# Performance work log

Hardware: AMD Instinct MI355X
Metric: run time of the kernel (lower is better)

The kernel has to match this reference:

```python
import jax, jax.numpy as jnp
import numpy as np

H, W = 256, 256
N = 1024          # num gaussians
K = 4             # num clusters
M = 50            # num components
ALPHA_THRESH = 1.0 / 255.0
ALPHA_CLAMP = 0.999


def setup_inputs() -> dict:
    key = jax.random.key(0)
    k1, k2, k3 = jax.random.split(key, 3)
    # torch init: atanh(2*(rand-0.5)); keep away from +-1 for finite atanh
    u = jax.random.uniform(k1, (N, 2), minval=0.01, maxval=0.99)
    xyz_raw = jnp.arctanh(2.0 * (u - 0.5))
    cholesky_raw = jax.random.uniform(k2, (N, 3))
    opacity = jnp.ones((N, 1), jnp.float32)
    features_dc = jax.random.uniform(k3, (K, M, N, 3))
    return {"xyz_raw": xyz_raw, "cholesky_raw": cholesky_raw,
            "opacity": opacity, "features_dc": features_dc, "cluster_id": 0}


def _gaussian_weights(xyz_raw, cholesky_raw, opacity):
    """Dense equivalent of project_gaussians_2d + rasterize_gaussians_sum weights.
    Returns [H*W, N] per-pixel per-gaussian alpha."""
    xy = jnp.tanh(xyz_raw)                                  # [N,2] in (-1,1)
    chol = cholesky_raw + jnp.array([0.5, 0.0, 0.5], dtype=cholesky_raw.dtype)
    l1, l2, l3 = chol[:, 0], chol[:, 1], chol[:, 2]
    # cov = L L^T with L = [[l1,0],[l2,l3]]
    a = l1 * l1
    b = l1 * l2
    c = l2 * l2 + l3 * l3
    det = a * c - b * b
    conic1, conic2, conic3 = c / det, -b / det, a / det      # inverse covariance
    # ndc -> pixel centers (gsplat ndc2pix convention)
    cx = 0.5 * ((xy[:, 0] + 1.0) * W - 1.0)                  # [N]
    cy = 0.5 * ((xy[:, 1] + 1.0) * H - 1.0)
    px = jnp.arange(W, dtype=xyz_raw.dtype)
    py = jnp.arange(H, dtype=xyz_raw.dtype)
    pxf = jnp.tile(px, H)                                    # [H*W] x coord
    pyf = jnp.repeat(py, W)                                  # [H*W] y coord
    dx = cx[None, :] - pxf[:, None]                          # [H*W, N]
    dy = cy[None, :] - pyf[:, None]
    sigma = 0.5 * (conic1[None, :] * dx * dx + conic3[None, :] * dy * dy) \
            + conic2[None, :] * dx * dy
    alpha = jnp.minimum(ALPHA_CLAMP, opacity[:, 0][None, :] * jnp.exp(-sigma))
    valid = (sigma >= 0.0) & (alpha >= ALPHA_THRESH)
    return jnp.where(valid, alpha, 0.0)                      # [H*W, N]


def reference(xyz_raw, cholesky_raw, opacity, features_dc, cluster_id):
    wgt = _gaussian_weights(xyz_raw, cholesky_raw, opacity)  # [H*W, N]
    feats = features_dc[cluster_id]                          # [M, N, 3]
    # out_stack[m,c,h,w] = sum_n wgt[p,n] * feats[m,n,c]  (background=0, scale=1, shift=0)
    out = jnp.einsum('pn,mnc->mcp', wgt, feats)
    return out.reshape(M, 3, H, W)
```

## Files before the change

kernel.cpp:

```cpp
#include <hip/hip_runtime.h>
#include <hip/hip_bf16.h>


namespace {
constexpr int WID = 256, HEI = 256, NPIX = WID * HEI;
constexpr int NG = 1024;
constexpr int MREP = 50;
constexpr int MC = 150;
constexpr int MCCHUNK = 50;
constexpr int TLX = 64, TLY = 4;
constexpr int CCAP = 64;
constexpr int FP = 52;
}

struct GParam { float cx, cy, A, B, C3, op, rx, ry; };

__device__ __forceinline__ float ldf(const void* p, int i, bool isb) {
    if (isb) return __bfloat162float(((const __hip_bfloat16*)p)[i]);
    return ((const float*)p)[i];
}

__device__ __forceinline__ GParam compute_gparam(const void* xyz, const void* chol,
                                                 const void* opac, int n, bool isb) {
    GParam g;
    float l1 = ldf(chol, 3 * n + 0, isb) + 0.5f;
    float l2 = ldf(chol, 3 * n + 1, isb);
    float l3 = ldf(chol, 3 * n + 2, isb) + 0.5f;
    float a = l1 * l1;
    float b = l1 * l2;
    float c = l2 * l2 + l3 * l3;
    float det = a * c - b * b;
    float inv = 1.0f / det;
    g.A = c * inv;
    g.B = -b * inv;
    g.C3 = a * inv;
    float x0 = tanhf(ldf(xyz, 2 * n + 0, isb));
    float x1 = tanhf(ldf(xyz, 2 * n + 1, isb));
    g.cx = 0.5f * ((x0 + 1.0f) * (float)WID - 1.0f);
    g.cy = 0.5f * ((x1 + 1.0f) * (float)HEI - 1.0f);
    g.op = ldf(opac, n, isb);
    float smax = logf(255.0f * g.op);
    if (smax > 0.0f) {
        g.rx = sqrtf(2.0f * smax * a) + 0.5f;
        g.ry = sqrtf(2.0f * smax * c) + 0.5f;
    } else {
        g.rx = -1.0f;
        g.ry = -1.0f;
    }
    return g;
}

__global__ __launch_bounds__(256) void prep_kernel(const void* __restrict__ xyz,
                                                   const void* __restrict__ chol,
                                                   const void* __restrict__ opac,
                                                   GParam* __restrict__ gp) {
    int n = blockIdx.x * 256 + threadIdx.x;
    if (n >= NG) return;
    bool isb = (((const unsigned*)opac)[0] == 0x3F803F80u);
    gp[n] = compute_gparam(xyz, chol, opac, n, isb);
}

__global__ __launch_bounds__(256) void raster_kernel(const GParam* __restrict__ gp,
                                                     const void* __restrict__ xyz,
                                                     const void* __restrict__ chol,
                                                     const void* __restrict__ opac,
                                                     const void* __restrict__ feats,
                                                     const int* __restrict__ cluster,
                                                     void* __restrict__ out) {
    __shared__ unsigned short cand[NG];
    __shared__ int candCnt;
    __shared__ float pLDS[CCAP][8];
    __shared__ float featLDS[CCAP * FP];

    const bool isb = (((const unsigned*)opac)[0] == 0x3F803F80u);
    const int tid = threadIdx.x;
    const int tx0 = blockIdx.x * TLX;
    const int ty0 = blockIdx.y * TLY;
    const int mc0 = blockIdx.z * MCCHUNK;

    if (tid == 0) candCnt = 0;
    __syncthreads();

    for (int g = tid; g < NG; g += 256) {
        GParam gg = gp ? gp[g] : compute_gparam(xyz, chol, opac, g, isb);
        bool keep = (gg.rx >= 0.0f) &&
                    (gg.cx + gg.rx >= (float)tx0) && (gg.cx - gg.rx <= (float)(tx0 + TLX - 1)) &&
                    (gg.cy + gg.ry >= (float)ty0) && (gg.cy - gg.ry <= (float)(ty0 + TLY - 1));
        if (keep) {
            int slot = atomicAdd(&candCnt, 1);
            cand[slot] = (unsigned short)g;
        }
    }
    __syncthreads();
    const int C = candCnt;
    const int nStage = (C < CCAP) ? C : CCAP;

    if (tid < nStage) {
        int n = cand[tid];
        GParam gg = gp ? gp[n] : compute_gparam(xyz, chol, opac, n, isb);
        pLDS[tid][0] = gg.cx;
        pLDS[tid][1] = gg.cy;
        pLDS[tid][2] = gg.A;
        pLDS[tid][3] = gg.B;
        pLDS[tid][4] = gg.C3;
        pLDS[tid][5] = gg.op;
        pLDS[tid][6] = gg.ry;
        pLDS[tid][7] = 0.0f;
    }
    const int clus = cluster[0];
    const int fbase = clus * (MREP * NG * 3);
    for (int t = tid; t < nStage * FP; t += 256) {
        int il = t / FP;
        int q = t - il * FP;
        float v = 0.0f;
        if (q < MCCHUNK) {
            int mc = mc0 + q;
            int m = mc / 3, cch = mc - m * 3;
            int n = cand[il];
            v = ldf(feats, fbase + m * (NG * 3) + n * 3 + cch, isb);
        }
        featLDS[t] = v;
    }
    __syncthreads();

    const int lx = tid & 63, ly = tid >> 6;
    const float px = (float)(tx0 + lx);
    const float py = (float)(ty0 + ly);

    float acc[FP];
#pragma unroll
    for (int q = 0; q < FP; ++q) acc[q] = 0.0f;

    for (int j = 0; j < C; ++j) {
        float cx, cy, A, B, C3, op, ry;
        if (j < CCAP) {
            const float4* p4 = (const float4*)&pLDS[j][0];
            float4 u = p4[0], v = p4[1];
            cx = u.x; cy = u.y; A = u.z; B = u.w;
            C3 = v.x; op = v.y; ry = v.z;
        } else {
            GParam gg = gp ? gp[cand[j]] : compute_gparam(xyz, chol, opac, cand[j], isb);
            cx = gg.cx; cy = gg.cy; A = gg.A; B = gg.B; C3 = gg.C3; op = gg.op; ry = gg.ry;
        }
        float dy = cy - py;
        if (fabsf(dy) > ry) continue;
        float dx = cx - px;
        float sig = 0.5f * (A * dx * dx + C3 * dy * dy) + B * dx * dy;
        float al = fminf(0.999f, op * expf(-sig));
        bool valid = (sig >= 0.0f) && (al >= (1.0f / 255.0f));
        float am = valid ? al : 0.0f;
        if (__any(am != 0.0f)) {
            if (j < CCAP) {
                const float4* f4 = (const float4*)&featLDS[j * FP];
#pragma unroll
                for (int q4 = 0; q4 < FP / 4; ++q4) {
                    float4 f = f4[q4];
                    acc[4 * q4 + 0] += am * f.x;
                    acc[4 * q4 + 1] += am * f.y;
                    acc[4 * q4 + 2] += am * f.z;
                    acc[4 * q4 + 3] += am * f.w;
                }
            } else {
                int n = cand[j];
                for (int q = 0; q < MCCHUNK; ++q) {
                    int mc = mc0 + q;
                    int m = mc / 3, cch = mc - m * 3;
                    acc[q] += am * ldf(feats, fbase + m * (NG * 3) + n * 3 + cch, isb);
                }
            }
        }
    }

    const int pix = (ty0 + ly) * WID + tx0 + lx;
    if (isb) {
        __hip_bfloat16* o = (__hip_bfloat16*)out;
#pragma unroll
        for (int q = 0; q < MCCHUNK; ++q) o[(mc0 + q) * NPIX + pix] = __float2bfloat16(acc[q]);
    } else {
        float* o = (float*)out;
#pragma unroll
        for (int q = 0; q < MCCHUNK; ++q) o[(mc0 + q) * NPIX + pix] = acc[q];
    }
}

extern "C" void kernel_launch(void* const* d_in, const int* in_sizes, int n_in,
                              void* d_out, int out_size, void* d_ws, size_t ws_size,
                              hipStream_t stream) {
    const void* xyz = d_in[0];
    const void* chol = d_in[1];
    const void* opac = d_in[2];
    const void* feats = d_in[3];
    const int* cl = (const int*)d_in[4];
    (void)in_sizes; (void)n_in; (void)out_size;

    GParam* gp = nullptr;
    if (ws_size >= NG * sizeof(GParam)) {
        gp = (GParam*)d_ws;
        prep_kernel<<<dim3((NG + 255) / 256), 256, 0, stream>>>(xyz, chol, opac, gp);
    }
    dim3 grid(WID / TLX, HEI / TLY, MC / MCCHUNK);
    raster_kernel<<<grid, 256, 0, stream>>>(gp, xyz, chol, opac, feats, cl, d_out);
}
```

Measured before the change: 91.39 us.

## Stage candidates in LDS batches, batch alpha evaluation, and halve channel chunk

Replaces the single 64-candidate LDS stage plus slow global fallback with a loop that stages every candidate in batches of 64. Alpha is computed four gaussians at a time using fast __expf, and the early dy-based skip is dropped. The channel chunk per block shrinks from 50 to 25 (6 z-blocks), which cuts accumulator registers to raise occupancy. A template removes the runtime gp null check. The cost is that gaussian selection and parameter staging are now repeated across twice as many z-blocks.

Measured after the change: 87.93 us. -3.8%, faster.

```diff
diff --git a/kernel.cpp b/kernel.cpp
--- a/kernel.cpp
+++ b/kernel.cpp
@@ -7,10 +7,11 @@
 constexpr int NG = 1024;
 constexpr int MREP = 50;
 constexpr int MC = 150;
-constexpr int MCCHUNK = 50;
+constexpr int MCCHUNK = 25;
+constexpr int ZCH = 6;
 constexpr int TLX = 64, TLY = 4;
 constexpr int CCAP = 64;
-constexpr int FP = 52;
+constexpr int FP = 28;
 }
 
 struct GParam { float cx, cy, A, B, C3, op, rx, ry; };
@@ -60,6 +61,7 @@
     gp[n] = compute_gparam(xyz, chol, opac, n, isb);
 }
 
+template <bool HASGP>
 __global__ __launch_bounds__(256) void raster_kernel(const GParam* __restrict__ gp,
                                                      const void* __restrict__ xyz,
                                                      const void* __restrict__ chol,
@@ -82,7 +84,7 @@
     __syncthreads();
 
     for (int g = tid; g < NG; g += 256) {
-        GParam gg = gp ? gp[g] : compute_gparam(xyz, chol, opac, g, isb);
+        GParam gg = HASGP ? gp[g] : compute_gparam(xyz, chol, opac, g, isb);
         bool keep = (gg.rx >= 0.0f) &&
                     (gg.cx + gg.rx >= (float)tx0) && (gg.cx - gg.rx <= (float)(tx0 + TLX - 1)) &&
                     (gg.cy + gg.ry >= (float)ty0) && (gg.cy - gg.ry <= (float)(ty0 + TLY - 1));
@@ -93,36 +95,9 @@
     }
     __syncthreads();
     const int C = candCnt;
-    const int nStage = (C < CCAP) ? C : CCAP;
-
-    if (tid < nStage) {
-        int n = cand[tid];
-        GParam gg = gp ? gp[n] : compute_gparam(xyz, chol, opac, n, isb);
-        pLDS[tid][0] = gg.cx;
-        pLDS[tid][1] = gg.cy;
-        pLDS[tid][2] = gg.A;
-        pLDS[tid][3] = gg.B;
-        pLDS[tid][4] = gg.C3;
-        pLDS[tid][5] = gg.op;
-        pLDS[tid][6] = gg.ry;
-        pLDS[tid][7] = 0.0f;
-    }
+
     const int clus = cluster[0];
     const int fbase = clus * (MREP * NG * 3);
-    for (int t = tid; t < nStage * FP; t += 256) {
-        int il = t / FP;
-        int q = t - il * FP;
-        float v = 0.0f;
-        if (q < MCCHUNK) {
-            int mc = mc0 + q;
-            int m = mc / 3, cch = mc - m * 3;
-            int n = cand[il];
-            v = ldf(feats, fbase + m * (NG * 3) + n * 3 + cch, isb);
-        }
-        featLDS[t] = v;
-    }
-    __syncthreads();
-
     const int lx = tid & 63, ly = tid >> 6;
     const float px = (float)(tx0 + lx);
     const float py = (float)(ty0 + ly);
@@ -131,41 +106,64 @@
 #pragma unroll
     for (int q = 0; q < FP; ++q) acc[q] = 0.0f;
 
-    for (int j = 0; j < C; ++j) {
-        float cx, cy, A, B, C3, op, ry;
-        if (j < CCAP) {
-            const float4* p4 = (const float4*)&pLDS[j][0];
-            float4 u = p4[0], v = p4[1];
-            cx = u.x; cy = u.y; A = u.z; B = u.w;
-            C3 = v.x; op = v.y; ry = v.z;
-        } else {
-            GParam gg = gp ? gp[cand[j]] : compute_gparam(xyz, chol, opac, cand[j], isb);
-            cx = gg.cx; cy = gg.cy; A = gg.A; B = gg.B; C3 = gg.C3; op = gg.op; ry = gg.ry;
-        }
-        float dy = cy - py;
-        if (fabsf(dy) > ry) continue;
-        float dx = cx - px;
-        float sig = 0.5f * (A * dx * dx + C3 * dy * dy) + B * dx * dy;
-        float al = fminf(0.999f, op * expf(-sig));
-        bool valid = (sig >= 0.0f) && (al >= (1.0f / 255.0f));
-        float am = valid ? al : 0.0f;
-        if (__any(am != 0.0f)) {
-            if (j < CCAP) {
-                const float4* f4 = (const float4*)&featLDS[j * FP];
-#pragma unroll
-                for (int q4 = 0; q4 < FP / 4; ++q4) {
-                    float4 f = f4[q4];
-                    acc[4 * q4 + 0] += am * f.x;
-                    acc[4 * q4 + 1] += am * f.y;
-                    acc[4 * q4 + 2] += am * f.z;
-                    acc[4 * q4 + 3] += am * f.w;
+    for (int base = 0; base < C; base += CCAP) {
+        const int nStage = (C - base < CCAP) ? (C - base) : CCAP;
+        __syncthreads();
+        if (tid < nStage) {
+            int n = cand[base + tid];
+            GParam gg = HASGP ? gp[n] : compute_gparam(xyz, chol, opac, n, isb);
+            pLDS[tid][0] = gg.cx;
+            pLDS[tid][1] = gg.cy;
+            pLDS[tid][2] = gg.A;
+            pLDS[tid][3] = gg.B;
+            pLDS[tid][4] = gg.C3;
+            pLDS[tid][5] = gg.op;
+            pLDS[tid][6] = gg.ry;
+            pLDS[tid][7] = 0.0f;
+        }
+        for (int t = tid; t < nStage * FP; t += 256) {
+            int il = t / FP;
+            int q = t - il * FP;
+            float v = 0.0f;
+            if (q < MCCHUNK) {
+                int mc = mc0 + q;
+                int m = mc / 3, cch = mc - m * 3;
+                int n = cand[base + il];
+                v = ldf(feats, fbase + m * (NG * 3) + n * 3 + cch, isb);
+            }
+            featLDS[t] = v;
+        }
+        __syncthreads();
+
+        for (int jb = 0; jb < nStage; jb += 4) {
+            const int nj = nStage - jb;
+            float amv[4] = {0.0f, 0.0f, 0.0f, 0.0f};
+#pragma unroll
+            for (int k = 0; k < 4; ++k) {
+                if (k < nj) {
+                    const float4* p4 = (const float4*)&pLDS[jb + k][0];
+                    float4 u = p4[0], v = p4[1];
+                    float dx = u.x - px;
+                    float dy = u.y - py;
+                    float sig = 0.5f * (u.z * dx * dx + v.x * dy * dy) + u.w * dx * dy;
+                    float al = fminf(0.999f, v.y * __expf(-sig));
+                    bool valid = (sig >= 0.0f) && (al >= (1.0f / 255.0f));
+                    amv[k] = valid ? al : 0.0f;
                 }
-            } else {
-                int n = cand[j];
-                for (int q = 0; q < MCCHUNK; ++q) {
-                    int mc = mc0 + q;
-                    int m = mc / 3, cch = mc - m * 3;
-                    acc[q] += am * ldf(feats, fbase + m * (NG * 3) + n * 3 + cch, isb);
+            }
+#pragma unroll
+            for (int k = 0; k < 4; ++k) {
+                if (k < nj && __any(amv[k] != 0.0f)) {
+                    const float am = amv[k];
+                    const float4* f4 = (const float4*)&featLDS[(jb + k) * FP];
+#pragma unroll
+                    for (int q4 = 0; q4 < FP / 4; ++q4) {
+                        float4 f = f4[q4];
+                        acc[4 * q4 + 0] += am * f.x;
+                        acc[4 * q4 + 1] += am * f.y;
+                        acc[4 * q4 + 2] += am * f.z;
+                        acc[4 * q4 + 3] += am * f.w;
+                    }
                 }
             }
         }
@@ -193,11 +191,15 @@
     const int* cl = (const int*)d_in[4];
     (void)in_sizes; (void)n_in; (void)out_size;
 
-    GParam* gp = nullptr;
-    if (ws_size >= NG * sizeof(GParam)) {
-        gp = (GParam*)d_ws;
+    const bool hasgp = (ws_size >= NG * sizeof(GParam));
+    GParam* gp = hasgp ? (GParam*)d_ws : nullptr;
+    if (hasgp) {
         prep_kernel<<<dim3((NG + 255) / 256), 256, 0, stream>>>(xyz, chol, opac, gp);
     }
-    dim3 grid(WID / TLX, HEI / TLY, MC / MCCHUNK);
-    raster_kernel<<<grid, 256, 0, stream>>>(gp, xyz, chol, opac, feats, cl, d_out);
-}
+    dim3 grid(WID / TLX, HEI / TLY, ZCH);
+    if (hasgp) {
+        raster_kernel<true><<<grid, 256, 0, stream>>>(gp, xyz, chol, opac, feats, cl, d_out);
+    } else {
+        raster_kernel<false><<<grid, 256, 0, stream>>>(gp, xyz, chol, opac, feats, cl, d_out);
+    }
+}
```

## Drop LDS staging, read params/features via scalar loads, split channels into six chunks

Applied to the files above, without the earlier changes.

Removes the shared-memory staging of candidate parameters and features and instead reads each candidate's parameters and feature values straight from global memory, using a wave-uniform index via readfirstlane so the loads can be scalar. It halves the channel chunk per block (more blocks along z), removes the early ry cull, switches to fast __expf, and templates the kernel on whether the precomputed params exist. This cuts LDS footprint and sync overhead and raises occupancy, at the cost of per-candidate global/scalar loads that rely on caching and of strided feature reads.

After: 130.1 us. +42.3%, slower.

```diff
diff --git a/kernel.cpp b/kernel.cpp
--- a/kernel.cpp
+++ b/kernel.cpp
@@ -7,10 +7,9 @@
 constexpr int NG = 1024;
 constexpr int MREP = 50;
 constexpr int MC = 150;
-constexpr int MCCHUNK = 50;
+constexpr int MCCHUNK = 25;
+constexpr int ZCH = 6;
 constexpr int TLX = 64, TLY = 4;
-constexpr int CCAP = 64;
-constexpr int FP = 52;
 }
 
 struct GParam { float cx, cy, A, B, C3, op, rx, ry; };
@@ -18,6 +17,10 @@
 __device__ __forceinline__ float ldf(const void* p, int i, bool isb) {
     if (isb) return __bfloat162float(((const __hip_bfloat16*)p)[i]);
     return ((const float*)p)[i];
+}
+
+__device__ __forceinline__ bool is_bf16(const void* opac) {
+    return ((const unsigned*)opac)[0] == 0x3F803F80u;
 }
 
 __device__ __forceinline__ GParam compute_gparam(const void* xyz, const void* chol,
@@ -50,123 +53,82 @@
     return g;
 }
 
-__global__ __launch_bounds__(256) void prep_kernel(const void* __restrict__ xyz,
+__global__ __launch_bounds__(256) void prep_params(const void* __restrict__ xyz,
                                                    const void* __restrict__ chol,
                                                    const void* __restrict__ opac,
                                                    GParam* __restrict__ gp) {
     int n = blockIdx.x * 256 + threadIdx.x;
     if (n >= NG) return;
-    bool isb = (((const unsigned*)opac)[0] == 0x3F803F80u);
-    gp[n] = compute_gparam(xyz, chol, opac, n, isb);
+    gp[n] = compute_gparam(xyz, chol, opac, n, is_bf16(opac));
 }
 
-__global__ __launch_bounds__(256) void raster_kernel(const GParam* __restrict__ gp,
-                                                     const void* __restrict__ xyz,
-                                                     const void* __restrict__ chol,
-                                                     const void* __restrict__ opac,
-                                                     const void* __restrict__ feats,
-                                                     const int* __restrict__ cluster,
-                                                     void* __restrict__ out) {
+template <bool HASGP>
+__global__ __launch_bounds__(256) void raster(const GParam* __restrict__ gp,
+                                              const void* __restrict__ xyz,
+                                              const void* __restrict__ chol,
+                                              const void* __restrict__ opac,
+                                              const void* __restrict__ feats,
+                                              const int* __restrict__ cluster,
+                                              void* __restrict__ out) {
     __shared__ unsigned short cand[NG];
-    __shared__ int candCnt;
-    __shared__ float pLDS[CCAP][8];
-    __shared__ float featLDS[CCAP * FP];
+    __shared__ int cnt;
 
-    const bool isb = (((const unsigned*)opac)[0] == 0x3F803F80u);
+    const bool isb = is_bf16(opac);
     const int tid = threadIdx.x;
+    const int lx = tid & 63, ly = tid >> 6;
     const int tx0 = blockIdx.x * TLX;
     const int ty0 = blockIdx.y * TLY;
-    const int mc0 = blockIdx.z * MCCHUNK;
+    const int z = blockIdx.z;
+    const int mc0 = z * MCCHUNK;
+    const float px = (float)(tx0 + lx);
+    const float py = (float)(ty0 + ly);
 
-    if (tid == 0) candCnt = 0;
+    if (tid == 0) cnt = 0;
     __syncthreads();
 
-    for (int g = tid; g < NG; g += 256) {
-        GParam gg = gp ? gp[g] : compute_gparam(xyz, chol, opac, g, isb);
-        bool keep = (gg.rx >= 0.0f) &&
-                    (gg.cx + gg.rx >= (float)tx0) && (gg.cx - gg.rx <= (float)(tx0 + TLX - 1)) &&
-                    (gg.cy + gg.ry >= (float)ty0) && (gg.cy - gg.ry <= (float)(ty0 + TLY - 1));
-        if (keep) {
-            int slot = atomicAdd(&candCnt, 1);
-            cand[slot] = (unsigned short)g;
+    {
+        const float x0 = (float)tx0, y0 = (float)ty0;
+        const float x1 = x0 + (float)(TLX - 1), y1 = y0 + (float)(TLY - 1);
+        for (int g = tid; g < NG; g += 256) {
+            GParam gg = HASGP ? gp[g] : compute_gparam(xyz, chol, opac, g, isb);
+            bool keep = (gg.rx >= 0.0f) &&
+                        (gg.cx + gg.rx >= x0) && (gg.cx - gg.rx <= x1) &&
+                        (gg.cy + gg.ry >= y0) && (gg.cy - gg.ry <= y1);
+            if (keep) {
+                int s = atomicAdd(&cnt, 1);
+                cand[s] = (unsigned short)g;
+            }
         }
     }
     __syncthreads();
-    const int C = candCnt;
-    const int nStage = (C < CCAP) ? C : CCAP;
+    const int C = __builtin_amdgcn_readfirstlane(cnt);
 
-    if (tid < nStage) {
-        int n = cand[tid];
-        GParam gg = gp ? gp[n] : compute_gparam(xyz, chol, opac, n, isb);
-        pLDS[tid][0] = gg.cx;
-        pLDS[tid][1] = gg.cy;
-        pLDS[tid][2] = gg.A;
-        pLDS[tid][3] = gg.B;
-        pLDS[tid][4] = gg.C3;
-        pLDS[tid][5] = gg.op;
-        pLDS[tid][6] = gg.ry;
-        pLDS[tid][7] = 0.0f;
-    }
-    const int clus = cluster[0];
-    const int fbase = clus * (MREP * NG * 3);
-    for (int t = tid; t < nStage * FP; t += 256) {
-        int il = t / FP;
-        int q = t - il * FP;
-        float v = 0.0f;
-        if (q < MCCHUNK) {
-            int mc = mc0 + q;
-            int m = mc / 3, cch = mc - m * 3;
-            int n = cand[il];
-            v = ldf(feats, fbase + m * (NG * 3) + n * 3 + cch, isb);
-        }
-        featLDS[t] = v;
-    }
-    __syncthreads();
+    const int fbase = cluster[0] * (MREP * NG * 3);
 
-    const int lx = tid & 63, ly = tid >> 6;
-    const float px = (float)(tx0 + lx);
-    const float py = (float)(ty0 + ly);
-
-    float acc[FP];
+    float acc[MCCHUNK];
 #pragma unroll
-    for (int q = 0; q < FP; ++q) acc[q] = 0.0f;
+    for (int q = 0; q < MCCHUNK; ++q) acc[q] = 0.0f;
 
     for (int j = 0; j < C; ++j) {
-        float cx, cy, A, B, C3, op, ry;
-        if (j < CCAP) {
-            const float4* p4 = (const float4*)&pLDS[j][0];
-            float4 u = p4[0], v = p4[1];
-            cx = u.x; cy = u.y; A = u.z; B = u.w;
-            C3 = v.x; op = v.y; ry = v.z;
+        const int n = __builtin_amdgcn_readfirstlane((int)cand[j]);
+        GParam g;
+        if (HASGP) {
+            g = gp[n];
         } else {
-            GParam gg = gp ? gp[cand[j]] : compute_gparam(xyz, chol, opac, cand[j], isb);
-            cx = gg.cx; cy = gg.cy; A = gg.A; B = gg.B; C3 = gg.C3; op = gg.op; ry = gg.ry;
+            g = compute_gparam(xyz, chol, opac, n, isb);
         }
-        float dy = cy - py;
-        if (fabsf(dy) > ry) continue;
-        float dx = cx - px;
-        float sig = 0.5f * (A * dx * dx + C3 * dy * dy) + B * dx * dy;
-        float al = fminf(0.999f, op * expf(-sig));
-        bool valid = (sig >= 0.0f) && (al >= (1.0f / 255.0f));
-        float am = valid ? al : 0.0f;
+        float dx = g.cx - px;
+        float dy = g.cy - py;
+        float sig = 0.5f * (g.A * dx * dx + g.C3 * dy * dy) + g.B * dx * dy;
+        float al = fminf(0.999f, g.op * __expf(-sig));
+        float am = (sig >= 0.0f && al >= (1.0f / 255.0f)) ? al : 0.0f;
         if (__any(am != 0.0f)) {
-            if (j < CCAP) {
-                const float4* f4 = (const float4*)&featLDS[j * FP];
 #pragma unroll
-                for (int q4 = 0; q4 < FP / 4; ++q4) {
-                    float4 f = f4[q4];
-                    acc[4 * q4 + 0] += am * f.x;
-                    acc[4 * q4 + 1] += am * f.y;
-                    acc[4 * q4 + 2] += am * f.z;
-                    acc[4 * q4 + 3] += am * f.w;
-                }
-            } else {
-                int n = cand[j];
-                for (int q = 0; q < MCCHUNK; ++q) {
-                    int mc = mc0 + q;
-                    int m = mc / 3, cch = mc - m * 3;
-                    acc[q] += am * ldf(feats, fbase + m * (NG * 3) + n * 3 + cch, isb);
-                }
+            for (int q = 0; q < MCCHUNK; ++q) {
+                int mc = mc0 + q;
+                int m = mc / 3, cch = mc - m * 3;
+                float fv = ldf(feats, fbase + m * (NG * 3) + n * 3 + cch, isb);
+                acc[q] += am * fv;
             }
         }
     }
@@ -193,11 +155,12 @@
     const int* cl = (const int*)d_in[4];
     (void)in_sizes; (void)n_in; (void)out_size;
 
-    GParam* gp = nullptr;
+    dim3 grid(WID / TLX, HEI / TLY, ZCH);
     if (ws_size >= NG * sizeof(GParam)) {
-        gp = (GParam*)d_ws;
-        prep_kernel<<<dim3((NG + 255) / 256), 256, 0, stream>>>(xyz, chol, opac, gp);
+        GParam* gp = (GParam*)d_ws;
+        prep_params<<<dim3((NG + 255) / 256), 256, 0, stream>>>(xyz, chol, opac, gp);
+        raster<true><<<grid, 256, 0, stream>>>(gp, xyz, chol, opac, feats, cl, d_out);
+    } else {
+        raster<false><<<grid, 256, 0, stream>>>(nullptr, xyz, chol, opac, feats, cl, d_out);
     }
-    dim3 grid(WID / TLX, HEI / TLY, MC / MCCHUNK);
-    raster_kernel<<<grid, 256, 0, stream>>>(gp, xyz, chol, opac, feats, cl, d_out);
 }
```
